# Performance work log

Measured on AMD Instinct MI355X. Metric: run time of the kernel, lower is better.

Reference implementation:

```python
import jax, jax.numpy as jnp
import numpy as np

D, P = 50, 2          # feature dim and max polynomial order (module defaults)
N = 32768             # batch size

def _indexset(d, p):
    # faithful numpy port of indexset(): all multi-indices of total order exactly p
    if d == 1:
        return np.full((1, 1), p, dtype=np.int64)
    blocks = []
    for i in range(p + 1):
        sub = _indexset(d - 1, p - i)
        blocks.append(np.concatenate([np.full((sub.shape[0], 1), i, np.int64), sub], axis=1))
    return np.concatenate(blocks, axis=0)

def _normal_basis(p):
    # faithful numpy port of NormalBasis(): (physicists') Hermite recurrence coefficients
    B = np.zeros((p + 1, p + 1), np.float32)
    B[0, 0] = 1.0
    if p >= 1:
        B[1, 1] = 2.0
    for i in range(1, p):
        B[i + 1, 1:i + 2] = 2.0 * B[i, :i + 1]
        B[i + 1, :i] -= 2.0 * i * B[i - 1, :i]
    return B

def setup_inputs() -> dict:
    key = jax.random.key(0)
    k1, k2 = jax.random.split(key)
    x = jax.random.normal(k1, (N, D), dtype=jnp.float32)
    mean = jax.random.normal(k2, (D,), dtype=jnp.float32)
    var = jnp.ones((D,), dtype=jnp.float32)  # divisor; ones keeps values well-scaled
    oneDbasis = jnp.asarray(_normal_basis(P))                                   # (P+1, P+1)
    idxset = jnp.asarray(np.concatenate([_indexset(D, i) for i in range(P + 1)], axis=0))  # (1326, 50)
    return {"x": x, "mean": mean, "var": var, "oneDbasis": oneDbasis, "idxset": idxset}

def reference(x, mean, var, oneDbasis, idxset):
    p1 = oneDbasis.shape[0]  # p + 1
    # per-dim normalization (original mutates x in place; same math)
    xn = (x - mean) / var                                        # (n, d)
    # PolyVal: powers 0..p then weighted sum over basis coefficients
    x_pows = xn[..., None] ** jnp.arange(p1, dtype=xn.dtype)     # (n, d, p+1)
    polyval = jnp.einsum('ndi,pi->ndp', x_pows, oneDbasis)       # (n, d, p+1)
    n = x.shape[0]
    nbasis = idxset.shape[0]
    # Phi *= polyval[:, j, idxset[:, j]] accumulated over the d feature dims
    def body(Phi, xs):
        pv_j, idx_j = xs                 # pv_j: (n, p+1), idx_j: (nbasis,)
        return Phi * pv_j[:, idx_j], None
    Phi, _ = jax.lax.scan(body,
                          jnp.ones((n, nbasis), dtype=x.dtype),
                          (jnp.transpose(polyval, (1, 0, 2)), idxset.T))
    return Phi
```

## Files before the change

### kernel.cpp

```cpp
#include <hip/hip_runtime.h>


#define DD     50
#define P1     3
#define NBASIS 1326
#define BN     8
#define BLOCK  256

__global__ void build_desc_kernel(const int* __restrict__ idxset,
                                  int* __restrict__ desc, int nbasis, int d) {
    int b = blockIdx.x * blockDim.x + threadIdx.x;
    if (b >= nbasis) return;
    const int* row = idxset + (size_t)b * d;
    int off0 = 0, off1 = 0, cnt = 0;
    for (int j = 0; j < d; ++j) {
        int o = row[j];
        if (o != 0) {
            int off = j * P1 + o;
            if (cnt == 0) off0 = off; else off1 = off;
            ++cnt;
        }
    }
    desc[b] = off0 | (off1 << 8);
}

__global__ __launch_bounds__(BLOCK) void pce_kernel(
    const float* __restrict__ x, const float* __restrict__ mean,
    const float* __restrict__ var, const float* __restrict__ basis,
    const int* __restrict__ desc, float* __restrict__ out, int n)
{
    __shared__ float s_pv[BN][DD * P1];
    __shared__ int   s_desc[NBASIS];
    const int tid  = threadIdx.x;
    const int row0 = blockIdx.x * BN;

    for (int i = tid; i < NBASIS; i += BLOCK) s_desc[i] = desc[i];

    float b00 = basis[0], b01 = basis[1], b02 = basis[2];
    float b10 = basis[3], b11 = basis[4], b12 = basis[5];
    float b20 = basis[6], b21 = basis[7], b22 = basis[8];

    for (int i = tid; i < BN * DD; i += BLOCK) {
        int r = i / DD, c = i - r * DD;
        int row = row0 + r;
        if (row < n) {
            float xv = (x[(size_t)row * DD + c] - mean[c]) / var[c];
            float x2 = xv * xv;
            s_pv[r][c * P1 + 0] = b00 + b01 * xv + b02 * x2;
            s_pv[r][c * P1 + 1] = b10 + b11 * xv + b12 * x2;
            s_pv[r][c * P1 + 2] = b20 + b21 * xv + b22 * x2;
        }
    }
    __syncthreads();

    #pragma unroll
    for (int r = 0; r < BN; ++r) {
        int row = row0 + r;
        if (row >= n) break;
        const float* pvr = s_pv[r];
        float2* orow = (float2*)(out + (size_t)row * NBASIS);
        for (int b2 = tid; b2 < NBASIS / 2; b2 += BLOCK) {
            int d0 = s_desc[2 * b2];
            int d1 = s_desc[2 * b2 + 1];
            float2 v;
            v.x = pvr[d0 & 0xff] * pvr[(d0 >> 8) & 0xff];
            v.y = pvr[d1 & 0xff] * pvr[(d1 >> 8) & 0xff];
            orow[b2] = v;
        }
    }
}

extern "C" void kernel_launch(void* const* d_in, const int* in_sizes, int n_in,
                              void* d_out, int out_size, void* d_ws, size_t ws_size,
                              hipStream_t stream) {
    const float* x     = (const float*)d_in[0];
    const float* mean  = (const float*)d_in[1];
    const float* var   = (const float*)d_in[2];
    const float* basis = (const float*)d_in[3];
    const int*   idxset= (const int*)d_in[4];
    float* out = (float*)d_out;

    const int d      = in_sizes[1];
    const int n      = in_sizes[0] / d;
    const int nbasis = in_sizes[4] / d;

    int* desc = (int*)d_ws;
    build_desc_kernel<<<(nbasis + BLOCK - 1) / BLOCK, BLOCK, 0, stream>>>(idxset, desc, nbasis, d);
    pce_kernel<<<(n + BN - 1) / BN, BLOCK, 0, stream>>>(x, mean, var, basis, desc, out, n);
}
```

Measured before the change: 201.0 us.

## Keep basis descriptors in registers and double rows per block

Each thread now loads its three descriptor pairs straight into registers instead of staging all descriptors in shared memory, and fully unrolls the per-row output loop. Rows per block go from 8 to 16 to amortize setup, and the shared polyval rows get padding. Bounds checks on n are removed, so the kernel assumes n is a multiple of 16. This holds for the test size but would break other batch sizes.

```diff
diff --git a/kernel.cpp b/kernel.cpp
--- a/kernel.cpp
+++ b/kernel.cpp
@@ -4,7 +4,8 @@
 #define DD     50
 #define P1     3
 #define NBASIS 1326
-#define BN     8
+#define NPAIR  (NBASIS / 2)
+#define BN     16
 #define BLOCK  256
 
 __global__ void build_desc_kernel(const int* __restrict__ idxset,
@@ -29,43 +30,46 @@
     const float* __restrict__ var, const float* __restrict__ basis,
     const int* __restrict__ desc, float* __restrict__ out, int n)
 {
-    __shared__ float s_pv[BN][DD * P1];
-    __shared__ int   s_desc[NBASIS];
+    __shared__ float s_pv[BN][DD * P1 + 2];
     const int tid  = threadIdx.x;
     const int row0 = blockIdx.x * BN;
-
-    for (int i = tid; i < NBASIS; i += BLOCK) s_desc[i] = desc[i];
 
     float b00 = basis[0], b01 = basis[1], b02 = basis[2];
     float b10 = basis[3], b11 = basis[4], b12 = basis[5];
     float b20 = basis[6], b21 = basis[7], b22 = basis[8];
 
+    const int2* d2 = (const int2*)desc;
+    const int p0 = tid, p1 = tid + BLOCK, p2 = tid + 2 * BLOCK;
+    const bool has2 = (p2 < NPAIR);
+    int2 dA = d2[p0];
+    int2 dB = d2[p1];
+    int2 dC = has2 ? d2[p2] : make_int2(0, 0);
+
     for (int i = tid; i < BN * DD; i += BLOCK) {
         int r = i / DD, c = i - r * DD;
-        int row = row0 + r;
-        if (row < n) {
-            float xv = (x[(size_t)row * DD + c] - mean[c]) / var[c];
-            float x2 = xv * xv;
-            s_pv[r][c * P1 + 0] = b00 + b01 * xv + b02 * x2;
-            s_pv[r][c * P1 + 1] = b10 + b11 * xv + b12 * x2;
-            s_pv[r][c * P1 + 2] = b20 + b21 * xv + b22 * x2;
-        }
+        float xv = (x[(size_t)(row0 + r) * DD + c] - mean[c]) / var[c];
+        float x2 = xv * xv;
+        s_pv[r][c * P1 + 0] = b00 + b01 * xv + b02 * x2;
+        s_pv[r][c * P1 + 1] = b10 + b11 * xv + b12 * x2;
+        s_pv[r][c * P1 + 2] = b20 + b21 * xv + b22 * x2;
     }
     __syncthreads();
 
     #pragma unroll
     for (int r = 0; r < BN; ++r) {
-        int row = row0 + r;
-        if (row >= n) break;
         const float* pvr = s_pv[r];
-        float2* orow = (float2*)(out + (size_t)row * NBASIS);
-        for (int b2 = tid; b2 < NBASIS / 2; b2 += BLOCK) {
-            int d0 = s_desc[2 * b2];
-            int d1 = s_desc[2 * b2 + 1];
-            float2 v;
-            v.x = pvr[d0 & 0xff] * pvr[(d0 >> 8) & 0xff];
-            v.y = pvr[d1 & 0xff] * pvr[(d1 >> 8) & 0xff];
-            orow[b2] = v;
+        float2* orow = (float2*)(out + (size_t)(row0 + r) * NBASIS);
+        float2 v;
+        v.x = pvr[dA.x & 0xff] * pvr[dA.x >> 8];
+        v.y = pvr[dA.y & 0xff] * pvr[dA.y >> 8];
+        orow[p0] = v;
+        v.x = pvr[dB.x & 0xff] * pvr[dB.x >> 8];
+        v.y = pvr[dB.y & 0xff] * pvr[dB.y >> 8];
+        orow[p1] = v;
+        if (has2) {
+            v.x = pvr[dC.x & 0xff] * pvr[dC.x >> 8];
+            v.y = pvr[dC.y & 0xff] * pvr[dC.y >> 8];
+            orow[p2] = v;
         }
     }
 }
```

New measurement: 199.1 us. About the same (-1.0%).

## Precompute per-block float4 descriptors and emit contiguous nontemporal vector stores

Applied to the files above, without the earlier changes.

Each block of 4 rows now writes its 4*1326 outputs as one contiguous span of float4 stores. Every thread holds six register-resident int4 descriptors giving shared-memory offsets, built by a new precompute kernel with padded offsets (PERM) to reduce bank conflicts. The descriptor build is split into two kernels and the idxset is staged through shared memory. It also switches to nontemporal stores and removes row bounds checks, so it assumes n is a multiple of 4 and hardcodes the dimension constants.

```diff
diff --git a/kernel.cpp b/kernel.cpp
--- a/kernel.cpp
+++ b/kernel.cpp
@@ -1,90 +1,131 @@
 #include <hip/hip_runtime.h>
 
 
-#define DD     50
-#define P1     3
-#define NBASIS 1326
-#define BN     8
-#define BLOCK  256
+#define DD       50
+#define P1       3
+#define NBASIS   1326
+#define BN       4
+#define NQ       ((BN * NBASIS) / 4)
+#define BLOCK    256
+#define PVSTRIDE 192
+#define PERM(o)  ((o) + ((o) >> 2))
 
-__global__ void build_desc_kernel(const int* __restrict__ idxset,
-                                  int* __restrict__ desc, int nbasis, int d) {
-    int b = blockIdx.x * blockDim.x + threadIdx.x;
-    if (b >= nbasis) return;
-    const int* row = idxset + (size_t)b * d;
-    int off0 = 0, off1 = 0, cnt = 0;
-    for (int j = 0; j < d; ++j) {
-        int o = row[j];
-        if (o != 0) {
-            int off = j * P1 + o;
-            if (cnt == 0) off0 = off; else off1 = off;
-            ++cnt;
+typedef float vf4 __attribute__((ext_vector_type(4)));
+
+#define A1_ROWS 128
+__global__ __launch_bounds__(BLOCK) void build_compact(
+    const int* __restrict__ idxset, int* __restrict__ compact, int nbasis, int d)
+{
+    __shared__ int tile[A1_ROWS * DD];
+    const int r0   = blockIdx.x * A1_ROWS;
+    const int rows = min(A1_ROWS, nbasis - r0);
+    for (int i = threadIdx.x; i < rows * d; i += BLOCK)
+        tile[i] = idxset[(size_t)r0 * d + i];
+    __syncthreads();
+    const int r = threadIdx.x;
+    if (r < rows) {
+        const int* row = tile + r * d;
+        int off0 = 0, off1 = 0, cnt = 0;
+        for (int j = 0; j < d; ++j) {
+            int o = row[j];
+            if (o != 0) {
+                int off = j * P1 + o;
+                if (cnt == 0) off0 = off; else off1 = off;
+                ++cnt;
+            }
         }
+        compact[r0 + r] = off0 | (off1 << 8);
     }
-    desc[b] = off0 | (off1 << 8);
 }
 
-__global__ __launch_bounds__(BLOCK) void pce_kernel(
+__global__ __launch_bounds__(BLOCK) void build_desc4(
+    const int* __restrict__ compact, int4* __restrict__ desc4)
+{
+    int q = blockIdx.x * blockDim.x + threadIdx.x;
+    if (q >= NQ) return;
+    int w[4];
+    #pragma unroll
+    for (int k = 0; k < 4; ++k) {
+        int f  = 4 * q + k;
+        int rl = f / NBASIS;
+        int b  = f - rl * NBASIS;
+        int cb = compact[b];
+        int sA = rl * PVSTRIDE + PERM(cb & 0xff);
+        int sB = rl * PVSTRIDE + PERM((cb >> 8) & 0xff);
+        w[k] = sA | (sB << 16);
+    }
+    desc4[q] = make_int4(w[0], w[1], w[2], w[3]);
+}
+
+#define EMIT(d, ptr) do {                                              \
+    vf4 v;                                                             \
+    v.x = s_pv[(d).x & 0xffff] * s_pv[((unsigned)(d).x) >> 16];        \
+    v.y = s_pv[(d).y & 0xffff] * s_pv[((unsigned)(d).y) >> 16];        \
+    v.z = s_pv[(d).z & 0xffff] * s_pv[((unsigned)(d).z) >> 16];        \
+    v.w = s_pv[(d).w & 0xffff] * s_pv[((unsigned)(d).w) >> 16];        \
+    __builtin_nontemporal_store(v, (vf4*)(ptr));                       \
+} while (0)
+
+__global__ __launch_bounds__(BLOCK, 4) void pce4_kernel(
     const float* __restrict__ x, const float* __restrict__ mean,
     const float* __restrict__ var, const float* __restrict__ basis,
-    const int* __restrict__ desc, float* __restrict__ out, int n)
+    const int4* __restrict__ desc4, float* __restrict__ out)
 {
-    __shared__ float s_pv[BN][DD * P1];
-    __shared__ int   s_desc[NBASIS];
+    __shared__ float s_pv[BN * PVSTRIDE];
     const int tid  = threadIdx.x;
     const int row0 = blockIdx.x * BN;
 
-    for (int i = tid; i < NBASIS; i += BLOCK) s_desc[i] = desc[i];
+    int4 d0 = desc4[tid];
+    int4 d1 = desc4[tid + 256];
+    int4 d2 = desc4[tid + 512];
+    int4 d3 = desc4[tid + 768];
+    int4 d4 = desc4[tid + 1024];
+    const bool tail = (tid < NQ - 1280);
+    int4 d5 = tail ? desc4[tid + 1280] : make_int4(0, 0, 0, 0);
 
     float b00 = basis[0], b01 = basis[1], b02 = basis[2];
     float b10 = basis[3], b11 = basis[4], b12 = basis[5];
     float b20 = basis[6], b21 = basis[7], b22 = basis[8];
 
-    for (int i = tid; i < BN * DD; i += BLOCK) {
-        int r = i / DD, c = i - r * DD;
-        int row = row0 + r;
-        if (row < n) {
-            float xv = (x[(size_t)row * DD + c] - mean[c]) / var[c];
-            float x2 = xv * xv;
-            s_pv[r][c * P1 + 0] = b00 + b01 * xv + b02 * x2;
-            s_pv[r][c * P1 + 1] = b10 + b11 * xv + b12 * x2;
-            s_pv[r][c * P1 + 2] = b20 + b21 * xv + b22 * x2;
-        }
+    if (tid < BN * DD) {
+        int r = tid / DD, c = tid - r * DD;
+        float xv = (x[(size_t)row0 * DD + tid] - mean[c]) / var[c];
+        float x2 = xv * xv;
+        int base = r * PVSTRIDE;
+        s_pv[base + PERM(P1 * c + 0)] = b00 + b01 * xv + b02 * x2;
+        s_pv[base + PERM(P1 * c + 1)] = b10 + b11 * xv + b12 * x2;
+        s_pv[base + PERM(P1 * c + 2)] = b20 + b21 * xv + b22 * x2;
     }
     __syncthreads();
 
-    #pragma unroll
-    for (int r = 0; r < BN; ++r) {
-        int row = row0 + r;
-        if (row >= n) break;
-        const float* pvr = s_pv[r];
-        float2* orow = (float2*)(out + (size_t)row * NBASIS);
-        for (int b2 = tid; b2 < NBASIS / 2; b2 += BLOCK) {
-            int d0 = s_desc[2 * b2];
-            int d1 = s_desc[2 * b2 + 1];
-            float2 v;
-            v.x = pvr[d0 & 0xff] * pvr[(d0 >> 8) & 0xff];
-            v.y = pvr[d1 & 0xff] * pvr[(d1 >> 8) & 0xff];
-            orow[b2] = v;
-        }
-    }
+    vf4* obase = (vf4*)(out + (size_t)row0 * NBASIS);
+    EMIT(d0, obase + tid);
+    EMIT(d1, obase + tid + 256);
+    EMIT(d2, obase + tid + 512);
+    EMIT(d3, obase + tid + 768);
+    EMIT(d4, obase + tid + 1024);
+    if (tail) EMIT(d5, obase + tid + 1280);
 }
 
 extern "C" void kernel_launch(void* const* d_in, const int* in_sizes, int n_in,
                               void* d_out, int out_size, void* d_ws, size_t ws_size,
                               hipStream_t stream) {
-    const float* x     = (const float*)d_in[0];
-    const float* mean  = (const float*)d_in[1];
-    const float* var   = (const float*)d_in[2];
-    const float* basis = (const float*)d_in[3];
-    const int*   idxset= (const int*)d_in[4];
+    const float* x      = (const float*)d_in[0];
+    const float* mean   = (const float*)d_in[1];
+    const float* var    = (const float*)d_in[2];
+    const float* basis  = (const float*)d_in[3];
+    const int*   idxset = (const int*)d_in[4];
     float* out = (float*)d_out;
 
     const int d      = in_sizes[1];
     const int n      = in_sizes[0] / d;
     const int nbasis = in_sizes[4] / d;
 
-    int* desc = (int*)d_ws;
-    build_desc_kernel<<<(nbasis + BLOCK - 1) / BLOCK, BLOCK, 0, stream>>>(idxset, desc, nbasis, d);
-    pce_kernel<<<(n + BN - 1) / BN, BLOCK, 0, stream>>>(x, mean, var, basis, desc, out, n);
+    int*  compact = (int*)d_ws;
+    int4* desc4   = (int4*)((char*)d_ws + 8192);
+
+    build_compact<<<(nbasis + A1_ROWS - 1) / A1_ROWS, BLOCK, 0, stream>>>(
+        idxset, compact, nbasis, d);
+    build_desc4<<<(NQ + BLOCK - 1) / BLOCK, BLOCK, 0, stream>>>(compact, desc4);
+    pce4_kernel<<<n / BN, BLOCK, 0, stream>>>(x, mean, var, basis, desc4, out);
 }
```

Result: slower. 206.6 us (+2.8%).
